# Kernel optimization log

Measured on AMD Instinct MI355X. Metric: run time of the kernel, lower is better.

The kernel has to match this reference:

```python
import jax, jax.numpy as jnp
import numpy as np

SUB_NO = 20
T_NO = 201
E_NO = 2000
I_NO = 500
T_DATA = 20000

def _make_cden():
    C = np.zeros((SUB_NO, SUB_NO), dtype=np.float32)
    for i in range(SUB_NO):
        for c in (2 * i + 1, 2 * i + 2):
            if c < SUB_NO:
                C[i, c] = 1.0
    return C

C_DEN = _make_cden()
CHILDREN = [np.where(C_DEN[s] == 1)[0] for s in range(SUB_NO)]  # static tree structure


def setup_inputs() -> dict:
    key = jax.random.key(0)
    ks = jax.random.split(key, 12)
    eps = 1e-6
    inp = {}
    inp['S_e'] = jax.random.uniform(ks[0], (T_DATA, E_NO), dtype=jnp.float32)
    inp['S_i'] = jax.random.uniform(ks[1], (T_DATA, I_NO), dtype=jnp.float32)
    # uniform noise for REBAR reparam; clipped away from {0,1} so log(-log(u)) is finite
    inp['u'] = jnp.clip(jax.random.uniform(ks[2], (SUB_NO, E_NO + I_NO), dtype=jnp.float32), eps, 1.0 - eps)
    inp['v'] = jnp.clip(jax.random.uniform(ks[3], (SUB_NO, E_NO + I_NO), dtype=jnp.float32), eps, 1.0 - eps)
    inp['W_syn'] = jax.random.normal(ks[4], (SUB_NO, 2), dtype=jnp.float32) * 0.1
    inp['Tau_syn'] = jnp.ones((SUB_NO, 2), dtype=jnp.float32)
    inp['Delta_syn'] = jax.random.uniform(ks[5], (SUB_NO, 2), dtype=jnp.float32)
    inp['W_sub'] = jax.random.uniform(ks[6], (SUB_NO,), dtype=jnp.float32)
    inp['V_o'] = jax.random.normal(ks[7], (1,), dtype=jnp.float32)
    inp['Theta'] = jnp.zeros((SUB_NO,), dtype=jnp.float32)
    inp['C_syn_log'] = jnp.ones((SUB_NO, E_NO + I_NO), dtype=jnp.float32)
    return inp


def _H(x):
    # one-hot of per-column argmax (first max, as torch.argmax)
    idx = jnp.argmax(x, axis=0)
    return jax.nn.one_hot(idx, x.shape[0], axis=0, dtype=x.dtype)


def _reparam_pz(u, theta):
    return jnp.log(theta) - jnp.log(-jnp.log(u))


def _reparam_pz_b(v, b, theta):
    # b is one-hot per column; v_k = v at the b==1 row of each column
    v_k = jnp.sum(v * b, axis=0, keepdims=True)  # [1, cols]
    z_same = -jnp.log(-jnp.log(v))
    z_diff = -jnp.log(-jnp.log(v) / theta - jnp.log(v_k))
    return b * z_same + (1.0 - b) * z_diff


def _evaluate_f(C_syn, S_e, S_i, W_syn, Tau_syn, Delta_syn, W_sub, V_o):
    T_data = S_e.shape[0]
    C_syn_e = C_syn[:, :E_NO]          # [sub, E]
    C_syn_i = C_syn[:, -I_NO:]         # [sub, I]
    # double-exponential (alpha) synaptic kernels, vectorized over subunits & e/i
    t_raw = jnp.arange(T_NO, dtype=S_e.dtype)                               # [T_no]
    t = jnp.maximum(t_raw[None, None, :] - jnp.exp(Delta_syn)[:, :, None], 0.0)  # [sub,2,T_no]
    t_tau = t / jnp.exp(Tau_syn)[:, :, None]
    kern = t_tau * jnp.exp(-t_tau) * W_syn[:, :, None]                      # [sub,2,T_no]
    # project spikes onto subunits
    in_e = S_e @ C_syn_e.T   # [T, sub]
    in_i = S_i @ C_syn_i.T   # [T, sub]
    # causal depthwise conv: syn[t,s] = sum_tau kern[s,:,tau] * in[t-tau,s]
    inp = jnp.stack([in_e.T, in_i.T], axis=1).reshape(1, SUB_NO * 2, T_data)   # NCH
    k = jnp.flip(kern, axis=-1).reshape(SUB_NO * 2, 1, T_NO)                   # OIH
    filt = jax.lax.conv_general_dilated(
        inp, k, window_strides=(1,), padding=[(T_NO - 1, 0)],
        feature_group_count=SUB_NO * 2,
        dimension_numbers=('NCH', 'OIH', 'NCH'))
    syn_in = filt.reshape(SUB_NO, 2, T_data).sum(axis=1).T   # [T, sub]
    # tree-recurrent tanh aggregation (children have higher index than parents)
    sub_out = [None] * SUB_NO
    for s in range(SUB_NO):
        idx = SUB_NO - 1 - s
        ch = CHILDREN[idx]
        if ch.size == 0:
            sub_out[idx] = jnp.tanh(syn_in[:, idx])
        else:
            leaf = sum(sub_out[c] * W_sub[c] for c in ch)
            sub_out[idx] = jnp.tanh(syn_in[:, idx] + leaf)
    return sub_out[0] * W_sub[0] + V_o[0]


def reference(S_e, S_i, u, v, W_syn, Tau_syn, Delta_syn, W_sub, V_o, Theta, C_syn_log):
    theta = jax.nn.softmax(C_syn_log, axis=0)
    rebar_z = _reparam_pz(u, theta)
    hard_z = _H(rebar_z)
    rebar_zb = _reparam_pz_b(v, hard_z, theta)
    soft_z = jax.nn.sigmoid(rebar_z / 0.5) + 1e-9
    soft_zb = jax.nn.sigmoid(rebar_zb / 0.5) + 1e-9
    V_hard_z = _evaluate_f(hard_z, S_e, S_i, W_syn, Tau_syn, Delta_syn, W_sub, V_o)
    V_soft_z = _evaluate_f(soft_z, S_e, S_i, W_syn, Tau_syn, Delta_syn, W_sub, V_o)
    V_soft_zb = _evaluate_f(soft_zb, S_e, S_i, W_syn, Tau_syn, Delta_syn, W_sub, V_o)
    return (V_hard_z, V_soft_z, V_soft_zb, theta, hard_z, soft_z, soft_zb)
```

## Files before the change

kernel.cpp:

```cpp
#include <hip/hip_runtime.h>
#include <math.h>

#define SUBS 20
#define TAPS 201
#define ENO 2000
#define INO 500
#define TDATA 20000

typedef __bf16 bf16x8 __attribute__((ext_vector_type(8)));
typedef float f32x4 __attribute__((ext_vector_type(4)));

#define WGE_STRIDE 2048
#define WGI_STRIDE 512

#define WGE_OFF  0ull
#define WGI_OFF  262144ull
#define KERN_OFF 327680ull
#define INE_OFF  360448ull
#define INI_OFF  (INE_OFF + 4800000ull)
#define SYN_OFF  (INI_OFF + 4800000ull)
#define P2_OFF   (SYN_OFF + 4800000ull)
#define P3_OFF   (P2_OFF  + 4800000ull)
#define P4_OFF   (P3_OFF  + 4800000ull)

__device__ __forceinline__ unsigned short f2bf(float f) {
  union { float f; unsigned int u; } c; c.f = f;
  unsigned int u = c.u;
  return (unsigned short)((u + 0x7FFFu + ((u >> 16) & 1u)) >> 16);
}

__global__ __launch_bounds__(256) void prep_kernel(
    const float* __restrict__ u, const float* __restrict__ v,
    const float* __restrict__ C_log, const float* __restrict__ W_syn,
    const float* __restrict__ Tau_syn, const float* __restrict__ Delta_syn,
    float* __restrict__ out,
    unsigned short* __restrict__ wge, unsigned short* __restrict__ wgi,
    float* __restrict__ kern)
{
  if (blockIdx.x < 10) {
    const int n = blockIdx.x * 256 + threadIdx.x;
    if (n >= 2500) return;
    float x[SUBS], theta[SUBS], rebar[SUBS];
    float mx = -1e30f;
#pragma unroll
    for (int s = 0; s < SUBS; ++s) { x[s] = C_log[s*2500 + n]; mx = fmaxf(mx, x[s]); }
    float sum = 0.f;
#pragma unroll
    for (int s = 0; s < SUBS; ++s) { theta[s] = expf(x[s] - mx); sum += theta[s]; }
    const float inv = 1.f / sum;
    int idx = 0; float best = -1e30f;
#pragma unroll
    for (int s = 0; s < SUBS; ++s) {
      theta[s] *= inv;
      out[60000 + s*2500 + n] = theta[s];
      const float uu = u[s*2500 + n];
      const float r = logf(theta[s]) - logf(-logf(uu));
      rebar[s] = r;
      if (r > best) { best = r; idx = s; }
    }
    const float lvk = logf(v[idx*2500 + n]);
#pragma unroll
    for (int s = 0; s < SUBS; ++s) {
      const float hz = (s == idx) ? 1.f : 0.f;
      const float sz = 1.f / (1.f + expf(-2.f * rebar[s])) + 1e-9f;
      const float vv = v[s*2500 + n];
      const float zb = (s == idx) ? (-logf(-logf(vv)))
                                  : (-logf(-logf(vv) / theta[s] - lvk));
      const float szb = 1.f / (1.f + expf(-2.f * zb)) + 1e-9f;
      out[110000 + s*2500 + n] = hz;
      out[160000 + s*2500 + n] = sz;
      out[210000 + s*2500 + n] = szb;
      if (n < ENO) {
        wge[(s     )*WGE_STRIDE + n] = f2bf(hz);
        wge[(20 + s)*WGE_STRIDE + n] = f2bf(sz);
        wge[(40 + s)*WGE_STRIDE + n] = f2bf(szb);
      } else {
        const int k = n - ENO;
        wgi[(s     )*WGI_STRIDE + k] = f2bf(hz);
        wgi[(20 + s)*WGI_STRIDE + k] = f2bf(sz);
        wgi[(40 + s)*WGI_STRIDE + k] = f2bf(szb);
      }
    }
  } else {
    const int tid = threadIdx.x;
    for (int i = tid; i < 40*TAPS; i += 256) {
      const int ch = i / TAPS, m = i - ch*TAPS;
      const float dl  = expf(Delta_syn[ch]);
      const float tau = expf(Tau_syn[ch]);
      const float t  = fmaxf((float)m - dl, 0.f);
      const float tt = t / tau;
      kern[i] = tt * expf(-tt) * W_syn[ch];
    }
    for (int i = tid; i < 4*2048; i += 256) wge[(60 + (i >> 11))*WGE_STRIDE + (i & 2047)] = 0;
    for (int i = tid; i < 60*48;  i += 256) wge[(i / 48)*WGE_STRIDE + 2000 + (i % 48)] = 0;
    for (int i = tid; i < 4*512;  i += 256) wgi[(60 + (i >> 9))*WGI_STRIDE + (i & 511)] = 0;
    for (int i = tid; i < 60*12;  i += 256) wgi[(i / 12)*WGI_STRIDE + 500 + (i % 12)] = 0;
  }
}

__global__ __launch_bounds__(512) void gemm_kernel(
    const float* __restrict__ S_e, const float* __restrict__ S_i,
    const unsigned short* __restrict__ wge, const unsigned short* __restrict__ wgi,
    float* __restrict__ in_e, float* __restrict__ in_i,
    float* __restrict__ P1, float* __restrict__ P2,
    float* __restrict__ P3, float* __restrict__ P4)
{
  __shared__ unsigned short Alds[128*72];
  __shared__ unsigned short Blds[64*72];
  const int tid  = threadIdx.x;
  const int wave = tid >> 6;
  const int lane = tid & 63;
  const int m16  = lane & 15;
  const int quad = lane >> 4;
  const int t0   = blockIdx.x * 128;
  const int cy   = blockIdx.y;
  const bool isE = (cy < 4);

  const float* S = isE ? S_e : S_i;
  const unsigned short* Wg = isE ? wge : wgi;
  float* outp = (cy == 0) ? in_e : (cy == 1) ? P1 : (cy == 2) ? P2
              : (cy == 3) ? P3   : (cy == 4) ? in_i : P4;
  const int K       = isE ? ENO : INO;
  const int Wstride = isE ? WGE_STRIDE : WGI_STRIDE;
  const int k_base  = isE ? cy * 512 : (cy - 4) * 256;
  const int steps   = isE ? 8 : 4;

  const int rowA  = tid >> 2;
  const int slotA = tid & 3;
  const int rowB  = tid >> 3;
  const int slotB = tid & 7;
  const int tA    = t0 + rowA;
  const float* Arow = S + (size_t)((tA < TDATA) ? tA : TDATA - 1) * K;
  const unsigned short* Brow = Wg + (size_t)rowB * Wstride;

  f32x4 acc0 = {0.f,0.f,0.f,0.f};
  f32x4 acc1 = acc0, acc2 = acc0, acc3 = acc0;

  for (int st = 0; st < steps; ++st) {
    const int k0 = k_base + st * 64;
    const uint4 bw = *(const uint4*)(Brow + k0 + slotB*8);
    float4 v0, v1, v2, v3;
    {
      const int kb = k0 + slotA*16;
      const int c0 = (kb +  4 <= K) ? kb      : K - 4;
      const int c1 = (kb +  8 <= K) ? kb +  4 : K - 4;
      const int c2 = (kb + 12 <= K) ? kb +  8 : K - 4;
      const int c3 = (kb + 16 <= K) ? kb + 12 : K - 4;
      v0 = *(const float4*)(Arow + c0);
      v1 = *(const float4*)(Arow + c1);
      v2 = *(const float4*)(Arow + c2);
      v3 = *(const float4*)(Arow + c3);
    }
    ushort4 p0, p1, p2, p3;
    p0.x = f2bf(v0.x); p0.y = f2bf(v0.y); p0.z = f2bf(v0.z); p0.w = f2bf(v0.w);
    p1.x = f2bf(v1.x); p1.y = f2bf(v1.y); p1.z = f2bf(v1.z); p1.w = f2bf(v1.w);
    p2.x = f2bf(v2.x); p2.y = f2bf(v2.y); p2.z = f2bf(v2.z); p2.w = f2bf(v2.w);
    p3.x = f2bf(v3.x); p3.y = f2bf(v3.y); p3.z = f2bf(v3.z); p3.w = f2bf(v3.w);
    unsigned short* adst = &Alds[rowA*72 + slotA*16];
    *(ushort4*)(adst    ) = p0;  *(ushort4*)(adst + 4) = p1;
    *(ushort4*)(adst + 8) = p2;  *(ushort4*)(adst +12) = p3;
    *(uint4*)(&Blds[rowB*72 + slotB*8]) = bw;
    __syncthreads();
#pragma unroll
    for (int h = 0; h < 2; ++h) {
      const int kh = h*32 + quad*8;
      const bf16x8 a  = *(const bf16x8*)(&Alds[(wave*16 + m16)*72 + kh]);
      const bf16x8 b0 = *(const bf16x8*)(&Blds[(      m16)*72 + kh]);
      const bf16x8 b1 = *(const bf16x8*)(&Blds[(16 + m16)*72 + kh]);
      const bf16x8 b2 = *(const bf16x8*)(&Blds[(32 + m16)*72 + kh]);
      const bf16x8 b3 = *(const bf16x8*)(&Blds[(48 + m16)*72 + kh]);
      acc0 = __builtin_amdgcn_mfma_f32_16x16x32_bf16(a, b0, acc0, 0, 0, 0);
      acc1 = __builtin_amdgcn_mfma_f32_16x16x32_bf16(a, b1, acc1, 0, 0, 0);
      acc2 = __builtin_amdgcn_mfma_f32_16x16x32_bf16(a, b2, acc2, 0, 0, 0);
      acc3 = __builtin_amdgcn_mfma_f32_16x16x32_bf16(a, b3, acc3, 0, 0, 0);
    }
    __syncthreads();
  }
  const int t = t0 + wave*16 + quad*4;
  if (t < TDATA) {
    float* o = outp + t;
    *(float4*)(o + (size_t)(     m16)*TDATA) = *(float4*)&acc0;
    *(float4*)(o + (size_t)(16 + m16)*TDATA) = *(float4*)&acc1;
    *(float4*)(o + (size_t)(32 + m16)*TDATA) = *(float4*)&acc2;
    if (m16 < 12)
      *(float4*)(o + (size_t)(48 + m16)*TDATA) = *(float4*)&acc3;
  }
}

__global__ __launch_bounds__(256) void reduce_kernel(
    float* __restrict__ in_e, float* __restrict__ in_i,
    const float* __restrict__ P1, const float* __restrict__ P2,
    const float* __restrict__ P3, const float* __restrict__ P4)
{
  const int n4 = 60 * TDATA / 4;
  if (blockIdx.x >= 1172) {
    const int i = (blockIdx.x - 1172) * 256 + threadIdx.x;
    if (i < n4) {
      float4 a = ((const float4*)in_i)[i];
      const float4 p = ((const float4*)P4)[i];
      a.x += p.x; a.y += p.y; a.z += p.z; a.w += p.w;
      ((float4*)in_i)[i] = a;
    }
    return;
  }
  const int i = blockIdx.x * 256 + threadIdx.x;
  if (i < n4) {
    float4 a = ((const float4*)in_e)[i];
    const float4 p1 = ((const float4*)P1)[i];
    const float4 p2 = ((const float4*)P2)[i];
    const float4 p3 = ((const float4*)P3)[i];
    a.x += p1.x + p2.x + p3.x; a.y += p1.y + p2.y + p3.y;
    a.z += p1.z + p2.z + p3.z; a.w += p1.w + p2.w + p3.w;
    ((float4*)in_e)[i] = a;
  }
}

__device__ __forceinline__ int swz(int i) { return i + (i >> 5); }

__global__ __launch_bounds__(256) void conv_kernel(
    const float* __restrict__ in_e, const float* __restrict__ in_i,
    const float* __restrict__ kern, float* __restrict__ syn)
{
  __shared__ float Ee[2320];
  __shared__ float Ei[2320];
  const int ch = blockIdx.y;
  const int t0 = blockIdx.x * 2048;
  const int s  = ch % SUBS;
  const float* pe = in_e + (size_t)ch * TDATA;
  const float* pi = in_i + (size_t)ch * TDATA;
  for (int i = threadIdx.x; i < 2248; i += 256) {
    const int g = t0 - 200 + i;
    const bool ok = (g >= 0) && (g < TDATA);
    Ee[swz(i)] = ok ? pe[g] : 0.f;
    Ei[swz(i)] = ok ? pi[g] : 0.f;
  }
  __syncthreads();
  const float* ke = kern + (size_t)(s*2    ) * TAPS;
  const float* ki = kern + (size_t)(s*2 + 1) * TAPS;
  const int tb = threadIdx.x * 8;
  float acc[8] = {0.f,0.f,0.f,0.f,0.f,0.f,0.f,0.f};
  float we[8], wi[8];
#pragma unroll
  for (int j = 0; j < 8; ++j) {
    we[j] = Ee[swz(tb + 200 + j)];
    wi[j] = Ei[swz(tb + 200 + j)];
  }
#pragma unroll 8
  for (int m = 0; m < TAPS; ++m) {
    const float k0 = ke[m];
    const float k1 = ki[m];
#pragma unroll
    for (int j = 0; j < 8; ++j)
      acc[j] = fmaf(we[j], k0, fmaf(wi[j], k1, acc[j]));
    if (m < TAPS - 1) {
#pragma unroll
      for (int j = 7; j > 0; --j) { we[j] = we[j-1]; wi[j] = wi[j-1]; }
      we[0] = Ee[swz(tb + 199 - m)];
      wi[0] = Ei[swz(tb + 199 - m)];
    }
  }
  const int t = t0 + tb;
  if (t < TDATA) {
    float* o = syn + (size_t)ch * TDATA + t;
    *(float4*)(o    ) = make_float4(acc[0], acc[1], acc[2], acc[3]);
    *(float4*)(o + 4) = make_float4(acc[4], acc[5], acc[6], acc[7]);
  }
}

__global__ __launch_bounds__(256) void tree_kernel(
    const float* __restrict__ syn, const float* __restrict__ W_sub,
    const float* __restrict__ V_o, float* __restrict__ out)
{
  const int t = blockIdx.x * 256 + threadIdx.x;
  const int var = blockIdx.y;
  if (t >= TDATA) return;
  const float* sp = syn + (size_t)var * SUBS * TDATA + t;
  float so[SUBS];
#pragma unroll
  for (int s = SUBS - 1; s >= 0; --s) {
    float val = sp[(size_t)s * TDATA];
    const int c1 = 2*s + 1, c2 = 2*s + 2;
    if (c1 < SUBS) val += so[c1] * W_sub[c1];
    if (c2 < SUBS) val += so[c2] * W_sub[c2];
    so[s] = tanhf(val);
  }
  out[(size_t)var * TDATA + t] = so[0] * W_sub[0] + V_o[0];
}

extern "C" void kernel_launch(void* const* d_in, const int* in_sizes, int n_in,
                              void* d_out, int out_size, void* d_ws, size_t ws_size,
                              hipStream_t stream) {
  const float* S_e     = (const float*)d_in[0];
  const float* S_i     = (const float*)d_in[1];
  const float* u       = (const float*)d_in[2];
  const float* v       = (const float*)d_in[3];
  const float* W_syn   = (const float*)d_in[4];
  const float* Tau_syn = (const float*)d_in[5];
  const float* Delta   = (const float*)d_in[6];
  const float* W_sub   = (const float*)d_in[7];
  const float* V_o     = (const float*)d_in[8];
  const float* C_log   = (const float*)d_in[10];
  float* out = (float*)d_out;
  char* ws = (char*)d_ws;
  unsigned short* wge = (unsigned short*)(ws + WGE_OFF);
  unsigned short* wgi = (unsigned short*)(ws + WGI_OFF);
  float* kern = (float*)(ws + KERN_OFF);
  float* in_e = (float*)(ws + INE_OFF);
  float* in_i = (float*)(ws + INI_OFF);
  float* syn  = (float*)(ws + SYN_OFF);
  float* P1   = syn;
  float* P2   = (float*)(ws + P2_OFF);
  float* P3   = (float*)(ws + P3_OFF);
  float* P4   = (float*)(ws + P4_OFF);

  prep_kernel<<<dim3(11), dim3(256), 0, stream>>>(u, v, C_log, W_syn, Tau_syn,
                                                  Delta, out, wge, wgi, kern);
  gemm_kernel<<<dim3(157, 6), dim3(512), 0, stream>>>(
      S_e, S_i, wge, wgi, in_e, in_i, P1, P2, P3, P4);
  reduce_kernel<<<dim3(2344), dim3(256), 0, stream>>>(in_e, in_i, P1, P2, P3, P4);
  conv_kernel<<<dim3(10, 60), dim3(256), 0, stream>>>(in_e, in_i, kern, syn);
  tree_kernel<<<dim3(79, 3), dim3(256), 0, stream>>>(syn, W_sub, V_o, out);
}
```

Measured before the change: 345.5 us.

## Fuse split-K reduction into conv load and drop I-path split

Removes the separate reduce kernel: the conv kernel now sums the excitatory split-K partials while loading its LDS tile. The inhibitory GEMM runs as one K block instead of two, so its partial buffer goes away. Precise exp/log/tanh calls are swapped for fast intrinsics, which trades some accuracy for fewer instructions. Conv loads now read four arrays per element, including the halo region.

```diff
diff --git a/kernel.cpp b/kernel.cpp
--- a/kernel.cpp
+++ b/kernel.cpp
@@ -18,15 +18,22 @@
 #define KERN_OFF 327680ull
 #define INE_OFF  360448ull
 #define INI_OFF  (INE_OFF + 4800000ull)
-#define SYN_OFF  (INI_OFF + 4800000ull)
-#define P2_OFF   (SYN_OFF + 4800000ull)
+#define P1_OFF   (INI_OFF + 4800000ull)
+#define P2_OFF   (P1_OFF  + 4800000ull)
 #define P3_OFF   (P2_OFF  + 4800000ull)
-#define P4_OFF   (P3_OFF  + 4800000ull)
+#define SYN_OFF  (P3_OFF  + 4800000ull)
 
 __device__ __forceinline__ unsigned short f2bf(float f) {
   union { float f; unsigned int u; } c; c.f = f;
   unsigned int u = c.u;
   return (unsigned short)((u + 0x7FFFu + ((u >> 16) & 1u)) >> 16);
+}
+
+__device__ __forceinline__ float fast_tanh(float x) {
+  const float ax = fabsf(x);
+  const float e  = __expf(2.f * ax);
+  const float t  = 1.f - 2.f / (e + 1.f);
+  return copysignf(t, x);
 }
 
 __global__ __launch_bounds__(256) void prep_kernel(
@@ -46,7 +53,7 @@
     for (int s = 0; s < SUBS; ++s) { x[s] = C_log[s*2500 + n]; mx = fmaxf(mx, x[s]); }
     float sum = 0.f;
 #pragma unroll
-    for (int s = 0; s < SUBS; ++s) { theta[s] = expf(x[s] - mx); sum += theta[s]; }
+    for (int s = 0; s < SUBS; ++s) { theta[s] = __expf(x[s] - mx); sum += theta[s]; }
     const float inv = 1.f / sum;
     int idx = 0; float best = -1e30f;
 #pragma unroll
@@ -54,19 +61,19 @@
       theta[s] *= inv;
       out[60000 + s*2500 + n] = theta[s];
       const float uu = u[s*2500 + n];
-      const float r = logf(theta[s]) - logf(-logf(uu));
+      const float r = __logf(theta[s]) - __logf(-__logf(uu));
       rebar[s] = r;
       if (r > best) { best = r; idx = s; }
     }
-    const float lvk = logf(v[idx*2500 + n]);
+    const float lvk = __logf(v[idx*2500 + n]);
 #pragma unroll
     for (int s = 0; s < SUBS; ++s) {
       const float hz = (s == idx) ? 1.f : 0.f;
-      const float sz = 1.f / (1.f + expf(-2.f * rebar[s])) + 1e-9f;
+      const float sz = 1.f / (1.f + __expf(-2.f * rebar[s])) + 1e-9f;
       const float vv = v[s*2500 + n];
-      const float zb = (s == idx) ? (-logf(-logf(vv)))
-                                  : (-logf(-logf(vv) / theta[s] - lvk));
-      const float szb = 1.f / (1.f + expf(-2.f * zb)) + 1e-9f;
+      const float zb = (s == idx) ? (-__logf(-__logf(vv)))
+                                  : (-__logf(-__logf(vv) / theta[s] - lvk));
+      const float szb = 1.f / (1.f + __expf(-2.f * zb)) + 1e-9f;
       out[110000 + s*2500 + n] = hz;
       out[160000 + s*2500 + n] = sz;
       out[210000 + s*2500 + n] = szb;
@@ -85,11 +92,11 @@
     const int tid = threadIdx.x;
     for (int i = tid; i < 40*TAPS; i += 256) {
       const int ch = i / TAPS, m = i - ch*TAPS;
-      const float dl  = expf(Delta_syn[ch]);
-      const float tau = expf(Tau_syn[ch]);
+      const float dl  = __expf(Delta_syn[ch]);
+      const float tau = __expf(Tau_syn[ch]);
       const float t  = fmaxf((float)m - dl, 0.f);
       const float tt = t / tau;
-      kern[i] = tt * expf(-tt) * W_syn[ch];
+      kern[i] = tt * __expf(-tt) * W_syn[ch];
     }
     for (int i = tid; i < 4*2048; i += 256) wge[(60 + (i >> 11))*WGE_STRIDE + (i & 2047)] = 0;
     for (int i = tid; i < 60*48;  i += 256) wge[(i / 48)*WGE_STRIDE + 2000 + (i % 48)] = 0;
@@ -102,8 +109,7 @@
     const float* __restrict__ S_e, const float* __restrict__ S_i,
     const unsigned short* __restrict__ wge, const unsigned short* __restrict__ wgi,
     float* __restrict__ in_e, float* __restrict__ in_i,
-    float* __restrict__ P1, float* __restrict__ P2,
-    float* __restrict__ P3, float* __restrict__ P4)
+    float* __restrict__ P1, float* __restrict__ P2, float* __restrict__ P3)
 {
   __shared__ unsigned short Alds[128*72];
   __shared__ unsigned short Blds[64*72];
@@ -119,11 +125,11 @@
   const float* S = isE ? S_e : S_i;
   const unsigned short* Wg = isE ? wge : wgi;
   float* outp = (cy == 0) ? in_e : (cy == 1) ? P1 : (cy == 2) ? P2
-              : (cy == 3) ? P3   : (cy == 4) ? in_i : P4;
+              : (cy == 3) ? P3   : in_i;
   const int K       = isE ? ENO : INO;
   const int Wstride = isE ? WGE_STRIDE : WGI_STRIDE;
-  const int k_base  = isE ? cy * 512 : (cy - 4) * 256;
-  const int steps   = isE ? 8 : 4;
+  const int k_base  = isE ? cy * 512 : 0;
+  const int steps   = 8;
 
   const int rowA  = tid >> 2;
   const int slotA = tid & 3;
@@ -187,38 +193,12 @@
   }
 }
 
-__global__ __launch_bounds__(256) void reduce_kernel(
-    float* __restrict__ in_e, float* __restrict__ in_i,
-    const float* __restrict__ P1, const float* __restrict__ P2,
-    const float* __restrict__ P3, const float* __restrict__ P4)
-{
-  const int n4 = 60 * TDATA / 4;
-  if (blockIdx.x >= 1172) {
-    const int i = (blockIdx.x - 1172) * 256 + threadIdx.x;
-    if (i < n4) {
-      float4 a = ((const float4*)in_i)[i];
-      const float4 p = ((const float4*)P4)[i];
-      a.x += p.x; a.y += p.y; a.z += p.z; a.w += p.w;
-      ((float4*)in_i)[i] = a;
-    }
-    return;
-  }
-  const int i = blockIdx.x * 256 + threadIdx.x;
-  if (i < n4) {
-    float4 a = ((const float4*)in_e)[i];
-    const float4 p1 = ((const float4*)P1)[i];
-    const float4 p2 = ((const float4*)P2)[i];
-    const float4 p3 = ((const float4*)P3)[i];
-    a.x += p1.x + p2.x + p3.x; a.y += p1.y + p2.y + p3.y;
-    a.z += p1.z + p2.z + p3.z; a.w += p1.w + p2.w + p3.w;
-    ((float4*)in_e)[i] = a;
-  }
-}
-
 __device__ __forceinline__ int swz(int i) { return i + (i >> 5); }
 
 __global__ __launch_bounds__(256) void conv_kernel(
-    const float* __restrict__ in_e, const float* __restrict__ in_i,
+    const float* __restrict__ in_e, const float* __restrict__ P1,
+    const float* __restrict__ P2,  const float* __restrict__ P3,
+    const float* __restrict__ in_i,
     const float* __restrict__ kern, float* __restrict__ syn)
 {
   __shared__ float Ee[2320];
@@ -226,13 +206,16 @@
   const int ch = blockIdx.y;
   const int t0 = blockIdx.x * 2048;
   const int s  = ch % SUBS;
-  const float* pe = in_e + (size_t)ch * TDATA;
-  const float* pi = in_i + (size_t)ch * TDATA;
+  const size_t off = (size_t)ch * TDATA;
   for (int i = threadIdx.x; i < 2248; i += 256) {
     const int g = t0 - 200 + i;
-    const bool ok = (g >= 0) && (g < TDATA);
-    Ee[swz(i)] = ok ? pe[g] : 0.f;
-    Ei[swz(i)] = ok ? pi[g] : 0.f;
+    float e = 0.f, ii = 0.f;
+    if (g >= 0 && g < TDATA) {
+      e = in_e[off + g] + P1[off + g] + P2[off + g] + P3[off + g];
+      ii = in_i[off + g];
+    }
+    Ee[swz(i)] = e;
+    Ei[swz(i)] = ii;
   }
   __syncthreads();
   const float* ke = kern + (size_t)(s*2    ) * TAPS;
@@ -261,7 +244,7 @@
   }
   const int t = t0 + tb;
   if (t < TDATA) {
-    float* o = syn + (size_t)ch * TDATA + t;
+    float* o = syn + off + t;
     *(float4*)(o    ) = make_float4(acc[0], acc[1], acc[2], acc[3]);
     *(float4*)(o + 4) = make_float4(acc[4], acc[5], acc[6], acc[7]);
   }
@@ -282,7 +265,7 @@
     const int c1 = 2*s + 1, c2 = 2*s + 2;
     if (c1 < SUBS) val += so[c1] * W_sub[c1];
     if (c2 < SUBS) val += so[c2] * W_sub[c2];
-    so[s] = tanhf(val);
+    so[s] = fast_tanh(val);
   }
   out[(size_t)var * TDATA + t] = so[0] * W_sub[0] + V_o[0];
 }
@@ -307,17 +290,16 @@
   float* kern = (float*)(ws + KERN_OFF);
   float* in_e = (float*)(ws + INE_OFF);
   float* in_i = (float*)(ws + INI_OFF);
-  float* syn  = (float*)(ws + SYN_OFF);
-  float* P1   = syn;
+  float* P1   = (float*)(ws + P1_OFF);
   float* P2   = (float*)(ws + P2_OFF);
   float* P3   = (float*)(ws + P3_OFF);
-  float* P4   = (float*)(ws + P4_OFF);
+  float* syn  = (float*)(ws + SYN_OFF);
 
   prep_kernel<<<dim3(11), dim3(256), 0, stream>>>(u, v, C_log, W_syn, Tau_syn,
                                                   Delta, out, wge, wgi, kern);
-  gemm_kernel<<<dim3(157, 6), dim3(512), 0, stream>>>(
-      S_e, S_i, wge, wgi, in_e, in_i, P1, P2, P3, P4);
-  reduce_kernel<<<dim3(2344), dim3(256), 0, stream>>>(in_e, in_i, P1, P2, P3, P4);
-  conv_kernel<<<dim3(10, 60), dim3(256), 0, stream>>>(in_e, in_i, kern, syn);
+  gemm_kernel<<<dim3(157, 5), dim3(512), 0, stream>>>(
+      S_e, S_i, wge, wgi, in_e, in_i, P1, P2, P3);
+  conv_kernel<<<dim3(10, 60), dim3(256), 0, stream>>>(in_e, P1, P2, P3, in_i,
+                                                      kern, syn);
   tree_kernel<<<dim3(79, 3), dim3(256), 0, stream>>>(syn, W_sub, V_o, out);
 }
```

After: 337.2 us. -2.4%, faster.
